# Kernel optimization log

Measured on AMD Instinct MI355X. Metric: run time of the kernel, lower is better.

Reference implementation:

```python
import jax, jax.numpy as jnp
import numpy as np
import math

N = 50_000       # points (CSR segments)
V = 500_000      # mapped views (ragged rows)
IN_MAIN, IN_MAP, IN_MOD = 64, 16, 128
NC, NC_QK = 32, 8
EPS = 1e-12


def setup_inputs() -> dict:
    key = jax.random.key(0)
    ks = jax.random.split(key, 18)
    def rn(k, shape, fan_in=None):
        s = (1.0 / math.sqrt(fan_in)) if fan_in else 1.0
        return jax.random.normal(k, shape, jnp.float32) * s
    x_main = rn(ks[0], (N, IN_MAIN))
    x_mod = rn(ks[1], (V, IN_MOD))
    x_map = rn(ks[2], (V, IN_MAP))
    # CSR pointers: monotone, csr[0]=0, csr[-1]=V (full row coverage)
    inner = jnp.sort(jax.random.randint(ks[3], (N - 1,), 0, V))
    csr_idx = jnp.concatenate([jnp.zeros(1, jnp.int32), inner.astype(jnp.int32),
                               jnp.full((1,), V, jnp.int32)])
    return {
        "x_main": x_main, "x_mod": x_mod, "x_map": x_map, "csr_idx": csr_idx,
        # E_main: MLP([in_main, nc, nc], bias=False)
        "W_main1": rn(ks[4], (IN_MAIN, NC), IN_MAIN),
        "W_main2": rn(ks[5], (NC, NC), NC),
        # E_map (DeepSetFeat): elementwise MLP + segment-max set context + fuse
        "W_map1": rn(ks[6], (IN_MAP, NC), IN_MAP),
        "W_map2": rn(ks[7], (2 * NC, NC), 2 * NC),
        # E_mod: MLP([in_mod, in_mod, in_mod], bias=False)
        "W_mod1": rn(ks[8], (IN_MOD, IN_MOD), IN_MOD),
        "W_mod2": rn(ks[9], (IN_MOD, IN_MOD), IN_MOD),
        # Q, K linear heads (nc_inner -> nc_qk * num_groups), with bias
        "WQ": rn(ks[10], (NC, NC_QK), NC), "bQ": jnp.zeros((NC_QK,), jnp.float32),
        "WK": rn(ks[11], (NC, NC_QK), NC), "bK": jnp.zeros((NC_QK,), jnp.float32),
        # Gating(num_groups=1): weight init ones, bias init zeros
        "g_w": jnp.ones((1, 1), jnp.float32), "g_b": jnp.zeros((1, 1), jnp.float32),
    }


def reference(x_main, x_mod, x_map, csr_idx,
              W_main1, W_main2, W_map1, W_map2, W_mod1, W_mod2,
              WQ, bQ, WK, bK, g_w, g_b):
    counts = csr_idx[1:] - csr_idx[:-1]                     # [N]
    dense_idx = jnp.repeat(jnp.arange(N, dtype=jnp.int32), counts,
                           total_repeat_length=V)           # [V]
    nonempty = counts > 0                                   # [N]

    # --- encoders ---
    h_main = jax.nn.relu(x_main @ W_main1) @ W_main2        # [N, NC]
    h = jax.nn.relu(x_map @ W_map1)                         # [V, NC]
    set_ctx = jax.ops.segment_max(h, dense_idx, num_segments=N)
    set_ctx = jnp.where(nonempty[:, None], set_ctx, 0.0)    # empty segs -> 0
    h_map = jax.nn.relu(jnp.concatenate([h, set_ctx[dense_idx]], axis=1) @ W_map2)  # [V, NC]
    h_mod = jax.nn.relu(x_mod @ W_mod1) @ W_mod2            # [V, IN_MOD]

    # --- Q/K compatibilities (num_groups=1) ---
    keys = h_map @ WK + bK                                  # [V, NC_QK]
    queries = (h_main @ WQ + bQ)[dense_idx]                 # [V, NC_QK]
    comp = jnp.sum(keys * queries, axis=1) / jnp.sqrt(jnp.float32(NC_QK))  # [V]

    # --- segment_softmax_csr ---
    seg_max = jax.ops.segment_max(comp, dense_idx, num_segments=N)
    seg_max = jnp.where(nonempty, seg_max, 0.0)
    cexp = jnp.exp(comp - seg_max[dense_idx])               # [V]
    seg_sum = jax.ops.segment_sum(cexp, dense_idx, num_segments=N) + EPS
    att = cexp / seg_sum[dense_idx]                         # [V]

    # --- attention-weighted pooling ---
    x_pool = jax.ops.segment_sum(h_mod * att[:, None], dense_idx, num_segments=N)  # [N, IN_MOD]

    # --- gating on per-segment max compatibility ---
    gate_in = jnp.where(nonempty, seg_max, 0.0)[:, None]    # [N, 1]
    gate = jnp.tanh(jax.nn.relu(g_w * gate_in + g_b))       # [N, 1]
    x_pool = x_pool * gate

    x_seen = nonempty
    return x_pool, x_seen
```

## Files before the change

### kernel.cpp

```cpp
#include <hip/hip_runtime.h>
#include <math.h>

#define N_PTS 50000
#define V_VIEWS 500000
#define IN_MAIN 64
#define IN_MAP 16
#define IN_MOD 128
#define NC 32
#define NC_QK 8
#define SEG_EPS 1e-12f

#define KH_BLOCKS ((V_VIEWS + 63) / 64)
#define KA_BLOCKS ((N_PTS + 7) / 8)

typedef short bf16x8 __attribute__((ext_vector_type(8)));
typedef float f32x4 __attribute__((ext_vector_type(4)));

static __device__ __forceinline__ short f2bf(float x) {
    union { float f; unsigned u; } v; v.f = x;
    unsigned r = v.u + 0x7fffu + ((v.u >> 16) & 1u);
    return (short)(r >> 16);
}
static __device__ __forceinline__ float bf2f(unsigned short b) {
    union { unsigned u; float f; } v; v.u = ((unsigned)b) << 16; return v.f;
}


__global__ __launch_bounds__(256) void k0_setup(const int* __restrict__ csr,
                                                const float* __restrict__ Wmod1,
                                                const float* __restrict__ Wmod2,
                                                const float* __restrict__ Wm1,
                                                const float* __restrict__ Wm2,
                                                int* __restrict__ didx,
                                                float* __restrict__ pooled,
                                                float* __restrict__ ctxw,
                                                short* __restrict__ Wf,
                                                short* __restrict__ W1f,
                                                short* __restrict__ W2af,
                                                short* __restrict__ W2f) {
    int t = blockIdx.x * blockDim.x + threadIdx.x;
    int total = gridDim.x * blockDim.x;
    if (t < N_PTS) {
        int a = csr[t], b = csr[t + 1];
        for (int v = a; v < b; ++v) didx[v] = t;
    }
    for (int i = t; i < N_PTS * IN_MOD; i += total) pooled[i] = 0.f;
    for (int i = t; i < N_PTS * NC; i += total) ctxw[i] = 0.f;
    for (int i = t; i < IN_MOD * IN_MOD; i += total) {
        int e = i & 7, l = (i >> 3) & 63, j = (i >> 9) & 7, kk = i >> 12;
        int k = kk * 32 + ((l >> 4) << 3) + e;
        int ch = (j << 4) + (l & 15);
        Wf[i] = f2bf(Wmod1[k * IN_MOD + ch]);
        W2f[i] = f2bf(Wmod2[k * IN_MOD + ch]);
    }
    for (int i = t; i < 1024; i += total) {
        int e = i & 7, l = (i >> 3) & 63, j = i >> 9;
        int k = ((l >> 4) << 3) + e;
        int ch = (j << 4) + (l & 15);
        W1f[i] = (k < IN_MAP) ? f2bf(Wm1[k * NC + ch]) : (short)0;
        W2af[i] = f2bf(Wm2[k * NC + ch]);
    }
}

__global__ __launch_bounds__(256) void kHA(
    const float* __restrict__ x_map, const int* __restrict__ didx,
    const short* __restrict__ W1f, int* __restrict__ ctxbits,
    short* __restrict__ hbuf,
    const float* __restrict__ x_main, const float* __restrict__ W1,
    const float* __restrict__ W2, const float* __restrict__ WQ,
    const float* __restrict__ bQ, const float* __restrict__ WK,
    const float* __restrict__ bK,
    float* __restrict__ wq, float* __restrict__ qb) {
    __shared__ float hl[4][16 * 36];
    __shared__ float W1l[IN_MAIN * NC];
    __shared__ float W2l[NC * NC];
    __shared__ float WQl[NC * NC_QK];
    __shared__ float WKl[NC * NC_QK];
    __shared__ float bQl[NC_QK];
    __shared__ float bKl[NC_QK];
    __shared__ float h1buf[8][NC];
    __shared__ float h2buf[8][NC];
    __shared__ float qbuf[8][NC_QK];

    int tid = threadIdx.x;
    if (blockIdx.x < KH_BLOCKS) {
        int w = tid >> 6, lane = tid & 63;
        int vbase = blockIdx.x * 64 + w * 16;
        if (vbase >= V_VIEWS) return;
        const bf16x8* pW1 = (const bf16x8*)W1f;
        bf16x8 b1a = pW1[lane], b1b = pW1[64 + lane];

        bf16x8 a1 = (bf16x8){0, 0, 0, 0, 0, 0, 0, 0};
        if (lane < 32) {
            const float* xp = x_map + (size_t)(vbase + (lane & 15)) * IN_MAP + ((lane >> 4) << 3);
            float4 x0 = *(const float4*)xp;
            float4 x1 = *(const float4*)(xp + 4);
            a1[0] = f2bf(x0.x); a1[1] = f2bf(x0.y); a1[2] = f2bf(x0.z); a1[3] = f2bf(x0.w);
            a1[4] = f2bf(x1.x); a1[5] = f2bf(x1.y); a1[6] = f2bf(x1.z); a1[7] = f2bf(x1.w);
        }
        f32x4 d1a = (f32x4){0.f, 0.f, 0.f, 0.f}, d1b = (f32x4){0.f, 0.f, 0.f, 0.f};
        d1a = __builtin_amdgcn_mfma_f32_16x16x32_bf16(a1, b1a, d1a, 0, 0, 0);
        d1b = __builtin_amdgcn_mfma_f32_16x16x32_bf16(a1, b1b, d1b, 0, 0, 0);

        int c = lane & 15, kq = lane >> 4;
        int vr0 = kq << 2;
        float* hw = hl[w];
#pragma unroll
        for (int r = 0; r < 4; ++r) {
            hw[(vr0 + r) * 36 + c] = fmaxf(d1a[r], 0.f);
            hw[(vr0 + r) * 36 + c + 16] = fmaxf(d1b[r], 0.f);
        }
        const float* hr = hw + c * 36 + (kq << 3);
        float4 h0 = *(const float4*)hr;
        float4 h1 = *(const float4*)(hr + 4);
        bf16x8 a2;
        a2[0] = f2bf(h0.x); a2[1] = f2bf(h0.y); a2[2] = f2bf(h0.z); a2[3] = f2bf(h0.w);
        a2[4] = f2bf(h1.x); a2[5] = f2bf(h1.y); a2[6] = f2bf(h1.z); a2[7] = f2bf(h1.w);
        *(bf16x8*)(hbuf + (size_t)(vbase + c) * NC + (kq << 3)) = a2;

        int vg = vbase + vr0;
        int4 ss = *(const int4*)(didx + vg);
        const int* sp = (const int*)&ss;
        float ma = 0.f, mb = 0.f;
#pragma unroll
        for (int r = 0; r < 4; ++r) {
            ma = fmaxf(ma, fmaxf(d1a[r], 0.f));
            mb = fmaxf(mb, fmaxf(d1b[r], 0.f));
            bool runend = (r == 3) || (sp[r + 1] != sp[r]);
            if (runend) {
                atomicMax(&ctxbits[sp[r] * NC + c], __float_as_int(ma));
                atomicMax(&ctxbits[sp[r] * NC + c + 16], __float_as_int(mb));
                ma = 0.f; mb = 0.f;
            }
        }
    } else {
        int bid = blockIdx.x - KH_BLOCKS;
        for (int i = tid; i < IN_MAIN * NC; i += 256) W1l[i] = W1[i];
        for (int i = tid; i < NC * NC; i += 256) W2l[i] = W2[i];
        for (int i = tid; i < NC * NC_QK; i += 256) WQl[i] = WQ[i];
        for (int i = tid; i < NC * NC_QK; i += 256) WKl[i] = WK[i];
        if (tid < NC_QK) { bQl[tid] = bQ[tid]; bKl[tid] = bK[tid]; }
        __syncthreads();
        int g = tid >> 5, c = tid & 31;
        int p = bid * 8 + g;
        float h1 = 0.f;
        if (p < N_PTS) {
            const float* xr = x_main + (size_t)p * IN_MAIN;
            for (int k = 0; k < IN_MAIN; ++k) h1 += xr[k] * W1l[k * NC + c];
            h1 = fmaxf(h1, 0.f);
        }
        h1buf[g][c] = h1;
        __syncthreads();
        float h2 = 0.f;
        for (int j = 0; j < NC; ++j) h2 += h1buf[g][j] * W2l[j * NC + c];
        h2buf[g][c] = h2;
        __syncthreads();
        if (c < NC_QK) {
            float acc = bQl[c];
            for (int j = 0; j < NC; ++j) acc += h2buf[g][j] * WQl[j * NC_QK + c];
            qbuf[g][c] = acc;
        }
        __syncthreads();
        if (p < N_PTS) {
            float w = 0.f;
            for (int j = 0; j < NC_QK; ++j) w += WKl[c * NC_QK + j] * qbuf[g][j];
            wq[(size_t)p * NC + c] = w;
            if (c == 0) {
                float b = 0.f;
                for (int j = 0; j < NC_QK; ++j) b += bKl[j] * qbuf[g][j];
                qb[p] = b;
            }
        }
    }
}

__global__ __launch_bounds__(256) void kB2b_ctxw(
    const float* __restrict__ Wm2, float* __restrict__ ctxw) {
    __shared__ float W2bl[NC * NC];
    __shared__ float ctxl[8][NC];
    int tid = threadIdx.x;
    for (int i = tid; i < NC * NC; i += 256) W2bl[i] = Wm2[NC * NC + i];
    int g = tid >> 5, c = tid & 31;
    int s = blockIdx.x * 8 + g;
    float cv = (s < N_PTS) ? ctxw[(size_t)s * NC + c] : 0.f;
    ctxl[g][c] = cv;
    __syncthreads();
    if (s < N_PTS) {
        float val = 0.f;
        for (int j = 0; j < NC; ++j) val += ctxl[g][j] * W2bl[j * NC + c];
        ctxw[(size_t)s * NC + c] = val;
    }
}

__global__ __launch_bounds__(256) void kB3_comp(
    const short* __restrict__ hbuf, const int* __restrict__ didx,
    const short* __restrict__ W2af,
    const float* __restrict__ ctxW2b, const float* __restrict__ wq,
    const float* __restrict__ qb, float* __restrict__ comp) {
    int tid = threadIdx.x;
    int w = tid >> 6, lane = tid & 63;
    int vbase = blockIdx.x * 64 + w * 16;
    if (vbase >= V_VIEWS) return;
    const bf16x8* pW2 = (const bf16x8*)W2af;
    bf16x8 b2a = pW2[lane], b2b = pW2[64 + lane];
    int c = lane & 15, kq = lane >> 4;

    bf16x8 a2 = *(const bf16x8*)(hbuf + (size_t)(vbase + c) * NC + (kq << 3));
    f32x4 d2a = (f32x4){0.f, 0.f, 0.f, 0.f}, d2b = (f32x4){0.f, 0.f, 0.f, 0.f};
    d2a = __builtin_amdgcn_mfma_f32_16x16x32_bf16(a2, b2a, d2a, 0, 0, 0);
    d2b = __builtin_amdgcn_mfma_f32_16x16x32_bf16(a2, b2b, d2b, 0, 0, 0);

    int vr0 = kq << 2;
    int vg = vbase + vr0;
    int4 ss = *(const int4*)(didx + vg);
    const int* sp = (const int*)&ss;
    float part[4];
#pragma unroll
    for (int r = 0; r < 4; ++r) {
        size_t so = (size_t)sp[r] * NC;
        float m0 = fmaxf(d2a[r] + ctxW2b[so + c], 0.f);
        float m1 = fmaxf(d2b[r] + ctxW2b[so + c + 16], 0.f);
        part[r] = m0 * wq[so + c] + m1 * wq[so + c + 16];
    }
#pragma unroll
    for (int mask = 1; mask < 16; mask <<= 1) {
#pragma unroll
        for (int r = 0; r < 4; ++r) part[r] += __shfl_xor(part[r], mask);
    }
    if (c == 0) {
        const float inv_sqrt = 0.35355339059327373f;
        float4 o;
        o.x = (part[0] + qb[sp[0]]) * inv_sqrt;
        o.y = (part[1] + qb[sp[1]]) * inv_sqrt;
        o.z = (part[2] + qb[sp[2]]) * inv_sqrt;
        o.w = (part[3] + qb[sp[3]]) * inv_sqrt;
        *(float4*)(comp + vg) = o;
    }
}

__global__ __launch_bounds__(256) void kB4_att(
    const float* __restrict__ comp, const int* __restrict__ csr,
    float* __restrict__ segmax, float* __restrict__ invsum) {
    int wid = threadIdx.x >> 6, lane = threadIdx.x & 63;
    int seg = blockIdx.x * 4 + wid;
    if (seg >= N_PTS) return;
    int v0 = csr[seg], v1 = csr[seg + 1];
    if (v0 >= v1) {
        if (lane == 0) { segmax[seg] = 0.f; invsum[seg] = 0.f; }
        return;
    }
    float mx = -__builtin_inff();
    for (int v = v0 + lane; v < v1; v += 64) mx = fmaxf(mx, comp[v]);
    for (int o = 32; o > 0; o >>= 1) mx = fmaxf(mx, __shfl_xor(mx, o));
    float sm = 0.f;
    for (int v = v0 + lane; v < v1; v += 64) sm += __expf(comp[v] - mx);
    for (int o = 32; o > 0; o >>= 1) sm += __shfl_xor(sm, o);
    if (lane == 0) { segmax[seg] = mx; invsum[seg] = 1.f / (sm + SEG_EPS); }
}

#define VB 64
__global__ __launch_bounds__(256) void kC_pool(
    const float* __restrict__ x_mod, const short* __restrict__ Wf,
    const int* __restrict__ didx, const int* __restrict__ csr,
    const float* __restrict__ comp, const float* __restrict__ segmax,
    const float* __restrict__ invsum, float* __restrict__ pooled) {
    __shared__ unsigned short Ybl[VB * 136];
    __shared__ float attl[VB];
    __shared__ int didxl[VB];
    __shared__ int csrAl[VB];
    __shared__ int csrBl[VB];
    int tid = threadIdx.x;
    int vbase = blockIdx.x * VB;
    if (tid < VB) {
        int v = vbase + tid;
        if (v < V_VIEWS) {
            int s = didx[v];
            didxl[tid] = s;
            attl[tid] = __expf(comp[v] - segmax[s]) * invsum[s];
            csrAl[tid] = csr[s];
            csrBl[tid] = csr[s + 1];
        } else {
            int s = didx[V_VIEWS - 1];
            didxl[tid] = s;
            attl[tid] = 0.f;
            csrAl[tid] = csr[s];
            csrBl[tid] = csr[s + 1];
        }
    }
    __syncthreads();

    int w = tid >> 6, lane = tid & 63;
    int row16 = lane & 15;
    int kq = lane >> 4;
    int k0 = kq << 3;
    f32x4 acc[8];
    for (int j = 0; j < 8; ++j) acc[j] = (f32x4){0.f, 0.f, 0.f, 0.f};

    int v = vbase + w * 16 + row16;
    if (v >= V_VIEWS) v = V_VIEWS - 1;
    const float* xp = x_mod + (size_t)v * IN_MOD;

#pragma unroll
    for (int kk = 0; kk < 4; ++kk) {
        float4 x0 = *(const float4*)(xp + kk * 32 + k0);
        float4 x1 = *(const float4*)(xp + kk * 32 + k0 + 4);
        bf16x8 a;
        a[0] = f2bf(x0.x); a[1] = f2bf(x0.y); a[2] = f2bf(x0.z); a[3] = f2bf(x0.w);
        a[4] = f2bf(x1.x); a[5] = f2bf(x1.y); a[6] = f2bf(x1.z); a[7] = f2bf(x1.w);
        const bf16x8* wf = (const bf16x8*)(Wf + ((size_t)(kk * 8) * 64 + lane) * 8);
#pragma unroll
        for (int j = 0; j < 8; ++j) {
            bf16x8 b = wf[j * 64];
            acc[j] = __builtin_amdgcn_mfma_f32_16x16x32_bf16(a, b, acc[j], 0, 0, 0);
        }
    }
#pragma unroll
    for (int j = 0; j < 8; ++j) {
        int ch = j * 16 + row16;
        int rbase = w * 16 + (kq << 2);
#pragma unroll
        for (int r = 0; r < 4; ++r) {
            int rw = rbase + r;
            Ybl[rw * 136 + ch] = (unsigned short)f2bf(fmaxf(acc[j][r], 0.f) * attl[rw]);
        }
    }
    __syncthreads();
    {
        int halfid = tid >> 7, cc = tid & 127;
        int r0 = halfid << 5;
        int hb = vbase + r0;
        float s_acc = 0.f;
        int cur = didxl[r0];
        int curA = csrAl[r0], curB = csrBl[r0];
        for (int rc = 0; rc < 32; rc += 8) {
            float yv[8];
#pragma unroll
            for (int u = 0; u < 8; ++u) yv[u] = bf2f(Ybl[(r0 + rc + u) * 136 + cc]);
#pragma unroll
            for (int u = 0; u < 8; ++u) {
                int r = r0 + rc + u;
                int s = didxl[r];
                if (s != cur) {
                    if (curA >= hb && curB <= hb + 32)
                        pooled[(size_t)cur * IN_MOD + cc] = s_acc;
                    else
                        atomicAdd(&pooled[(size_t)cur * IN_MOD + cc], s_acc);
                    s_acc = 0.f; cur = s; curA = csrAl[r]; curB = csrBl[r];
                }
                s_acc += yv[u];
            }
        }
        if (curA >= hb && curB <= hb + 32)
            pooled[(size_t)cur * IN_MOD + cc] = s_acc;
        else
            atomicAdd(&pooled[(size_t)cur * IN_MOD + cc], s_acc);
    }
}

__global__ __launch_bounds__(256) void kD_final(
    const short* __restrict__ W2f,
    const float* __restrict__ segmax, const int* __restrict__ csr,
    const float* __restrict__ g_w, const float* __restrict__ g_b,
    float* __restrict__ out) {
    int tid = threadIdx.x;
    int w = tid >> 6, lane = tid & 63;
    int row16 = lane & 15;
    int kq = lane >> 4;
    int k0 = kq << 3;
    int rbase = blockIdx.x * 64 + w * 16;
    float gw = g_w[0], gb = g_b[0];

    int rr = rbase + row16;
    if (rr >= N_PTS) rr = N_PTS - 1;
    const float* xp = out + (size_t)rr * IN_MOD;

    f32x4 acc[8];
    for (int j = 0; j < 8; ++j) acc[j] = (f32x4){0.f, 0.f, 0.f, 0.f};
#pragma unroll
    for (int kk = 0; kk < 4; ++kk) {
        float4 x0 = *(const float4*)(xp + kk * 32 + k0);
        float4 x1 = *(const float4*)(xp + kk * 32 + k0 + 4);
        bf16x8 a;
        a[0] = f2bf(x0.x); a[1] = f2bf(x0.y); a[2] = f2bf(x0.z); a[3] = f2bf(x0.w);
        a[4] = f2bf(x1.x); a[5] = f2bf(x1.y); a[6] = f2bf(x1.z); a[7] = f2bf(x1.w);
        const bf16x8* wf = (const bf16x8*)(W2f + ((size_t)(kk * 8) * 64 + lane) * 8);
#pragma unroll
        for (int j = 0; j < 8; ++j) {
            bf16x8 b = wf[j * 64];
            acc[j] = __builtin_amdgcn_mfma_f32_16x16x32_bf16(a, b, acc[j], 0, 0, 0);
        }
    }
    float gate[4];
    int rowv[4];
#pragma unroll
    for (int r = 0; r < 4; ++r) {
        int ro = rbase + (kq << 2) + r;
        rowv[r] = ro;
        if (ro < N_PTS) {
            bool nz = csr[ro + 1] > csr[ro];
            float gin = nz ? segmax[ro] : 0.f;
            gate[r] = tanhf(fmaxf(gw * gin + gb, 0.f));
            if (row16 == 0) out[(size_t)N_PTS * IN_MOD + ro] = nz ? 1.f : 0.f;
        } else {
            gate[r] = 0.f;
        }
    }
#pragma unroll
    for (int j = 0; j < 8; ++j) {
        int ch = j * 16 + row16;
#pragma unroll
        for (int r = 0; r < 4; ++r) {
            if (rowv[r] < N_PTS)
                out[(size_t)rowv[r] * IN_MOD + ch] = acc[j][r] * gate[r];
        }
    }
}

extern "C" void kernel_launch(void* const* d_in, const int* in_sizes, int n_in,
                              void* d_out, int out_size, void* d_ws, size_t ws_size,
                              hipStream_t stream) {
    (void)in_sizes; (void)n_in; (void)out_size; (void)ws_size;
    const float* x_main = (const float*)d_in[0];
    const float* x_mod  = (const float*)d_in[1];
    const float* x_map  = (const float*)d_in[2];
    const int*   csr    = (const int*)d_in[3];
    const float* W_main1 = (const float*)d_in[4];
    const float* W_main2 = (const float*)d_in[5];
    const float* W_map1  = (const float*)d_in[6];
    const float* W_map2  = (const float*)d_in[7];
    const float* W_mod1  = (const float*)d_in[8];
    const float* W_mod2  = (const float*)d_in[9];
    const float* WQ = (const float*)d_in[10];
    const float* bQ = (const float*)d_in[11];
    const float* WK = (const float*)d_in[12];
    const float* bK = (const float*)d_in[13];
    const float* g_w = (const float*)d_in[14];
    const float* g_b = (const float*)d_in[15];
    float* out = (float*)d_out;

    char* ws = (char*)d_ws;
    int*   didx   = (int*)ws;
    float* wq     = (float*)(ws + 2000000);
    float* qb     = (float*)(ws + 8400000);
    float* ctxw   = (float*)(ws + 8600000);
    float* comp   = (float*)(ws + 15000000);
    float* segmax = (float*)(ws + 17000000);
    short* Wf     = (short*)(ws + 17200000);
    short* W1f    = (short*)(ws + 17240000);
    short* W2af   = (short*)(ws + 17244000);
    short* W2f    = (short*)(ws + 17248000);
    float* invsum = (float*)(ws + 17300000);
    short* hbuf   = (short*)(ws + 17500000);
    float* pooled = out;

    k0_setup<<<512, 256, 0, stream>>>(csr, W_mod1, W_mod2, W_map1, W_map2,
                                      didx, pooled, ctxw, Wf, W1f, W2af, W2f);
    kHA<<<KH_BLOCKS + KA_BLOCKS, 256, 0, stream>>>(x_map, didx, W1f, (int*)ctxw, hbuf,
                                                   x_main, W_main1, W_main2, WQ, bQ,
                                                   WK, bK, wq, qb);
    kB2b_ctxw<<<(N_PTS + 7) / 8, 256, 0, stream>>>(W_map2, ctxw);
    kB3_comp<<<(V_VIEWS + 63) / 64, 256, 0, stream>>>(hbuf, didx, W2af,
                                                      ctxw, wq, qb, comp);
    kB4_att<<<(N_PTS + 3) / 4, 256, 0, stream>>>(comp, csr, segmax, invsum);
    kC_pool<<<(V_VIEWS + VB - 1) / VB, 256, 0, stream>>>(x_mod, Wf, didx, csr,
                                                         comp, segmax, invsum, pooled);
    kD_final<<<(N_PTS + 63) / 64, 256, 0, stream>>>(W2f, segmax, csr, g_w, g_b, out);
}
```

Baseline: 221.6 us.

## Reduce set-context max in shared memory and shrink softmax segment groups

The segment-max set context in kHA is now first reduced into a per-block shared-memory table indexed by segment slot. It is then written to global memory with plain stores for segments fully inside the block, and with global atomics only for boundary segments. This replaces many per-wave global atomicMax operations. The kernel's shared memory is also unioned between its two branches to cut the LDS footprint. kB4_att now gives each segment 16 lanes instead of a 64-lane wave, which fits the average segment length of about 10 better but may serialize longer segments.

```diff
diff --git a/kernel.cpp b/kernel.cpp
--- a/kernel.cpp
+++ b/kernel.cpp
@@ -62,6 +62,21 @@
     }
 }
 
+struct KHsm {
+    float hl[4][16 * 36];
+    int ctxT[64 * 33];
+};
+struct KAsm {
+    float W1l[IN_MAIN * NC];
+    float W2l[NC * NC];
+    float WQl[NC * NC_QK];
+    float WKl[NC * NC_QK];
+    float bQl[NC_QK];
+    float bKl[NC_QK];
+    float h1buf[8][NC];
+    float h2buf[8][NC];
+    float qbuf[8][NC_QK];
+};
 __global__ __launch_bounds__(256) void kHA(
     const float* __restrict__ x_map, const int* __restrict__ didx,
     const short* __restrict__ W1f, int* __restrict__ ctxbits,
@@ -69,30 +84,27 @@
     const float* __restrict__ x_main, const float* __restrict__ W1,
     const float* __restrict__ W2, const float* __restrict__ WQ,
     const float* __restrict__ bQ, const float* __restrict__ WK,
-    const float* __restrict__ bK,
+    const float* __restrict__ bK, const int* __restrict__ csr,
     float* __restrict__ wq, float* __restrict__ qb) {
-    __shared__ float hl[4][16 * 36];
-    __shared__ float W1l[IN_MAIN * NC];
-    __shared__ float W2l[NC * NC];
-    __shared__ float WQl[NC * NC_QK];
-    __shared__ float WKl[NC * NC_QK];
-    __shared__ float bQl[NC_QK];
-    __shared__ float bKl[NC_QK];
-    __shared__ float h1buf[8][NC];
-    __shared__ float h2buf[8][NC];
-    __shared__ float qbuf[8][NC_QK];
-
+    __shared__ union { KHsm kh; KAsm ka; } sm;
     int tid = threadIdx.x;
     if (blockIdx.x < KH_BLOCKS) {
         int w = tid >> 6, lane = tid & 63;
-        int vbase = blockIdx.x * 64 + w * 16;
-        if (vbase >= V_VIEWS) return;
+        int vbb = blockIdx.x * 64;
+        int wend = (vbb + 64 < V_VIEWS) ? vbb + 64 : V_VIEWS;
+        int s_base = didx[vbb];
+        for (int i = tid; i < 64 * 33; i += 256) sm.kh.ctxT[i] = 0;
+        __syncthreads();
+
+        int vbase = vbb + w * 16;
         const bf16x8* pW1 = (const bf16x8*)W1f;
         bf16x8 b1a = pW1[lane], b1b = pW1[64 + lane];
 
         bf16x8 a1 = (bf16x8){0, 0, 0, 0, 0, 0, 0, 0};
         if (lane < 32) {
-            const float* xp = x_map + (size_t)(vbase + (lane & 15)) * IN_MAP + ((lane >> 4) << 3);
+            int vv = vbase + (lane & 15);
+            if (vv >= V_VIEWS) vv = V_VIEWS - 1;
+            const float* xp = x_map + (size_t)vv * IN_MAP + ((lane >> 4) << 3);
             float4 x0 = *(const float4*)xp;
             float4 x1 = *(const float4*)(xp + 4);
             a1[0] = f2bf(x0.x); a1[1] = f2bf(x0.y); a1[2] = f2bf(x0.z); a1[3] = f2bf(x0.w);
@@ -104,7 +116,7 @@
 
         int c = lane & 15, kq = lane >> 4;
         int vr0 = kq << 2;
-        float* hw = hl[w];
+        float* hw = sm.kh.hl[w];
 #pragma unroll
         for (int r = 0; r < 4; ++r) {
             hw[(vr0 + r) * 36 + c] = fmaxf(d1a[r], 0.f);
@@ -113,61 +125,83 @@
         const float* hr = hw + c * 36 + (kq << 3);
         float4 h0 = *(const float4*)hr;
         float4 h1 = *(const float4*)(hr + 4);
-        bf16x8 a2;
-        a2[0] = f2bf(h0.x); a2[1] = f2bf(h0.y); a2[2] = f2bf(h0.z); a2[3] = f2bf(h0.w);
-        a2[4] = f2bf(h1.x); a2[5] = f2bf(h1.y); a2[6] = f2bf(h1.z); a2[7] = f2bf(h1.w);
-        *(bf16x8*)(hbuf + (size_t)(vbase + c) * NC + (kq << 3)) = a2;
-
-        int vg = vbase + vr0;
-        int4 ss = *(const int4*)(didx + vg);
-        const int* sp = (const int*)&ss;
-        float ma = 0.f, mb = 0.f;
-#pragma unroll
-        for (int r = 0; r < 4; ++r) {
-            ma = fmaxf(ma, fmaxf(d1a[r], 0.f));
-            mb = fmaxf(mb, fmaxf(d1b[r], 0.f));
-            bool runend = (r == 3) || (sp[r + 1] != sp[r]);
-            if (runend) {
-                atomicMax(&ctxbits[sp[r] * NC + c], __float_as_int(ma));
-                atomicMax(&ctxbits[sp[r] * NC + c + 16], __float_as_int(mb));
-                ma = 0.f; mb = 0.f;
+        if (vbase + c < V_VIEWS) {
+            bf16x8 a2;
+            a2[0] = f2bf(h0.x); a2[1] = f2bf(h0.y); a2[2] = f2bf(h0.z); a2[3] = f2bf(h0.w);
+            a2[4] = f2bf(h1.x); a2[5] = f2bf(h1.y); a2[6] = f2bf(h1.z); a2[7] = f2bf(h1.w);
+            *(bf16x8*)(hbuf + (size_t)(vbase + c) * NC + (kq << 3)) = a2;
+        }
+        {
+            float ma = 0.f, mb = 0.f;
+            int pslot = -1;
+#pragma unroll
+            for (int r = 0; r < 4; ++r) {
+                int rw = vbase + vr0 + r;
+                if (rw < wend) {
+                    int slot = didx[rw] - s_base;
+                    if (slot != pslot) {
+                        if (pslot >= 0) {
+                            atomicMax(&sm.kh.ctxT[pslot * 33 + c], __float_as_int(ma));
+                            atomicMax(&sm.kh.ctxT[pslot * 33 + c + 16], __float_as_int(mb));
+                        }
+                        ma = 0.f; mb = 0.f; pslot = slot;
+                    }
+                    ma = fmaxf(ma, fmaxf(d1a[r], 0.f));
+                    mb = fmaxf(mb, fmaxf(d1b[r], 0.f));
+                }
             }
+            if (pslot >= 0) {
+                atomicMax(&sm.kh.ctxT[pslot * 33 + c], __float_as_int(ma));
+                atomicMax(&sm.kh.ctxT[pslot * 33 + c + 16], __float_as_int(mb));
+            }
+        }
+        __syncthreads();
+        int ns = didx[wend - 1] - s_base;
+        for (int idx = tid; idx < (ns + 1) * 32; idx += 256) {
+            int slot = idx >> 5, ch = idx & 31;
+            int bits = sm.kh.ctxT[slot * 33 + ch];
+            int s = s_base + slot;
+            bool interior = (csr[s] >= vbb) && (csr[s + 1] <= wend);
+            if (interior)
+                ((float*)ctxbits)[(size_t)s * NC + ch] = __int_as_float(bits);
+            else
+                atomicMax(&ctxbits[(size_t)s * NC + ch], bits);
         }
     } else {
         int bid = blockIdx.x - KH_BLOCKS;
-        for (int i = tid; i < IN_MAIN * NC; i += 256) W1l[i] = W1[i];
-        for (int i = tid; i < NC * NC; i += 256) W2l[i] = W2[i];
-        for (int i = tid; i < NC * NC_QK; i += 256) WQl[i] = WQ[i];
-        for (int i = tid; i < NC * NC_QK; i += 256) WKl[i] = WK[i];
-        if (tid < NC_QK) { bQl[tid] = bQ[tid]; bKl[tid] = bK[tid]; }
+        for (int i = tid; i < IN_MAIN * NC; i += 256) sm.ka.W1l[i] = W1[i];
+        for (int i = tid; i < NC * NC; i += 256) sm.ka.W2l[i] = W2[i];
+        for (int i = tid; i < NC * NC_QK; i += 256) sm.ka.WQl[i] = WQ[i];
+        for (int i = tid; i < NC * NC_QK; i += 256) sm.ka.WKl[i] = WK[i];
+        if (tid < NC_QK) { sm.ka.bQl[tid] = bQ[tid]; sm.ka.bKl[tid] = bK[tid]; }
         __syncthreads();
         int g = tid >> 5, c = tid & 31;
         int p = bid * 8 + g;
         float h1 = 0.f;
         if (p < N_PTS) {
             const float* xr = x_main + (size_t)p * IN_MAIN;
-            for (int k = 0; k < IN_MAIN; ++k) h1 += xr[k] * W1l[k * NC + c];
+            for (int k = 0; k < IN_MAIN; ++k) h1 += xr[k] * sm.ka.W1l[k * NC + c];
             h1 = fmaxf(h1, 0.f);
         }
-        h1buf[g][c] = h1;
+        sm.ka.h1buf[g][c] = h1;
         __syncthreads();
         float h2 = 0.f;
-        for (int j = 0; j < NC; ++j) h2 += h1buf[g][j] * W2l[j * NC + c];
-        h2buf[g][c] = h2;
+        for (int j = 0; j < NC; ++j) h2 += sm.ka.h1buf[g][j] * sm.ka.W2l[j * NC + c];
+        sm.ka.h2buf[g][c] = h2;
         __syncthreads();
         if (c < NC_QK) {
-            float acc = bQl[c];
-            for (int j = 0; j < NC; ++j) acc += h2buf[g][j] * WQl[j * NC_QK + c];
-            qbuf[g][c] = acc;
+            float acc = sm.ka.bQl[c];
+            for (int j = 0; j < NC; ++j) acc += sm.ka.h2buf[g][j] * sm.ka.WQl[j * NC_QK + c];
+            sm.ka.qbuf[g][c] = acc;
         }
         __syncthreads();
         if (p < N_PTS) {
             float w = 0.f;
-            for (int j = 0; j < NC_QK; ++j) w += WKl[c * NC_QK + j] * qbuf[g][j];
+            for (int j = 0; j < NC_QK; ++j) w += sm.ka.WKl[c * NC_QK + j] * sm.ka.qbuf[g][j];
             wq[(size_t)p * NC + c] = w;
             if (c == 0) {
                 float b = 0.f;
-                for (int j = 0; j < NC_QK; ++j) b += bKl[j] * qbuf[g][j];
+                for (int j = 0; j < NC_QK; ++j) b += sm.ka.bKl[j] * sm.ka.qbuf[g][j];
                 qb[p] = b;
             }
         }
@@ -241,21 +275,23 @@
 __global__ __launch_bounds__(256) void kB4_att(
     const float* __restrict__ comp, const int* __restrict__ csr,
     float* __restrict__ segmax, float* __restrict__ invsum) {
-    int wid = threadIdx.x >> 6, lane = threadIdx.x & 63;
-    int seg = blockIdx.x * 4 + wid;
+    int g16 = threadIdx.x >> 4, l16 = threadIdx.x & 15;
+    int seg = blockIdx.x * 16 + g16;
     if (seg >= N_PTS) return;
     int v0 = csr[seg], v1 = csr[seg + 1];
     if (v0 >= v1) {
-        if (lane == 0) { segmax[seg] = 0.f; invsum[seg] = 0.f; }
+        if (l16 == 0) { segmax[seg] = 0.f; invsum[seg] = 0.f; }
         return;
     }
     float mx = -__builtin_inff();
-    for (int v = v0 + lane; v < v1; v += 64) mx = fmaxf(mx, comp[v]);
-    for (int o = 32; o > 0; o >>= 1) mx = fmaxf(mx, __shfl_xor(mx, o));
+    for (int v = v0 + l16; v < v1; v += 16) mx = fmaxf(mx, comp[v]);
+#pragma unroll
+    for (int o = 8; o > 0; o >>= 1) mx = fmaxf(mx, __shfl_xor(mx, o, 16));
     float sm = 0.f;
-    for (int v = v0 + lane; v < v1; v += 64) sm += __expf(comp[v] - mx);
-    for (int o = 32; o > 0; o >>= 1) sm += __shfl_xor(sm, o);
-    if (lane == 0) { segmax[seg] = mx; invsum[seg] = 1.f / (sm + SEG_EPS); }
+    for (int v = v0 + l16; v < v1; v += 16) sm += __expf(comp[v] - mx);
+#pragma unroll
+    for (int o = 8; o > 0; o >>= 1) sm += __shfl_xor(sm, o, 16);
+    if (l16 == 0) { segmax[seg] = mx; invsum[seg] = 1.f / (sm + SEG_EPS); }
 }
 
 #define VB 64
@@ -457,11 +493,11 @@
                                       didx, pooled, ctxw, Wf, W1f, W2af, W2f);
     kHA<<<KH_BLOCKS + KA_BLOCKS, 256, 0, stream>>>(x_map, didx, W1f, (int*)ctxw, hbuf,
                                                    x_main, W_main1, W_main2, WQ, bQ,
-                                                   WK, bK, wq, qb);
+                                                   WK, bK, csr, wq, qb);
     kB2b_ctxw<<<(N_PTS + 7) / 8, 256, 0, stream>>>(W_map2, ctxw);
     kB3_comp<<<(V_VIEWS + 63) / 64, 256, 0, stream>>>(hbuf, didx, W2af,
                                                       ctxw, wq, qb, comp);
-    kB4_att<<<(N_PTS + 3) / 4, 256, 0, stream>>>(comp, csr, segmax, invsum);
+    kB4_att<<<(N_PTS + 15) / 16, 256, 0, stream>>>(comp, csr, segmax, invsum);
     kC_pool<<<(V_VIEWS + VB - 1) / VB, 256, 0, stream>>>(x_mod, Wf, didx, csr,
                                                          comp, segmax, invsum, pooled);
     kD_final<<<(N_PTS + 63) / 64, 256, 0, stream>>>(W2f, segmax, csr, g_w, g_b, out);
```

Result: faster. 208.4 us (-5.9%).
